# Kernel optimization log

Hardware: AMD Instinct MI355X
Metric: run time of the kernel (lower is better)

Reference implementation:

```python
import jax, jax.numpy as jnp
import numpy as np

VOCAB = 100000
PAD_ID = 0
INTEREST_ID = 1
B, S, D = 16, 200, 128

def setup_inputs() -> dict:
    key = jax.random.key(0)
    ks = jax.random.split(key, 10)
    sc = 0.05
    return {
        "x": jax.random.normal(ks[0], (B, S, D), jnp.float32),
        "x_ids": jax.random.randint(ks[1], (B, S), 0, VOCAB),
        "Wq": jax.random.normal(ks[2], (D, D), jnp.float32) * sc,
        "bq": jax.random.normal(ks[3], (D,), jnp.float32) * sc,
        "Wk": jax.random.normal(ks[4], (D, D), jnp.float32) * sc,
        "bk": jax.random.normal(ks[5], (D,), jnp.float32) * sc,
        "Wv": jax.random.normal(ks[6], (D, 1), jnp.float32) * sc,
        "bv": jax.random.normal(ks[7], (1,), jnp.float32) * sc,
        "Wec": jax.random.normal(ks[8], (2 * D, VOCAB), jnp.float32) * sc,
        "bec": jax.random.normal(ks[9], (VOCAB,), jnp.float32) * sc,
    }

def reference(x, x_ids, Wq, bq, Wk, bk, Wv, bv, Wec, bec):
    # mask: valid (non-pad, non-interest) positions  (B,S)
    mask = (x_ids != PAD_ID) & (x_ids != INTEREST_ID)
    # additive attention pooling (explore_proj=True)
    q = jnp.einsum('bsd,de->bse', x, Wq) + bq            # (B,S,D)
    k = jnp.einsum('bd,de->be', x[:, 0, :], Wk) + bk      # (B,D), broadcast over S
    features = jnp.tanh(q + k[:, None, :])                # (B,S,D)
    scores = jnp.einsum('bsd,do->bso', features, Wv)[..., 0] + bv[0]  # (B,S)
    scores = jax.nn.softmax(scores, axis=-1)
    c_s = jnp.einsum('bsd,bs->bd', x, scores)             # (B,D)
    h_t = x[:, 0, :]                                      # (B,D)
    c_s = jnp.concatenate([h_t, c_s], axis=-1)            # (B,2D)
    p_explore = c_s @ Wec + bec                           # (B,V)
    # explore_mask: histogram of masked ids over vocab.
    # Equivalent to bmm(mask, one_hot(x_ids)) but O(B*S) scatter instead of O(B*S*V).
    explore_mask = jnp.zeros((x.shape[0], VOCAB), jnp.float32)
    batch_idx = jnp.arange(x.shape[0])[:, None]           # (B,1)
    explore_mask = explore_mask.at[batch_idx, x_ids].add(mask.astype(jnp.float32))
    p_explore = jnp.where(explore_mask > 0, -jnp.inf, p_explore)
    return jax.nn.softmax(p_explore, axis=-1)
```

## Files before the change

### kernel.cpp

```cpp
#include <hip/hip_runtime.h>
#include <cstdint>
#include <cstddef>
#include <math.h>

#define B 16
#define S 200
#define D 128
#define VOCAB 100000
#define V4 (VOCAB / 4)
#define SCH 8
#define VTILE 256
#define NBLK ((VOCAB + VTILE - 1) / VTILE)
#define CH 16
#define NCH (2 * D / CH)

__global__ __launch_bounds__(128) void k_scores(
    const float* __restrict__ x,
    const float* __restrict__ Wq, const float* __restrict__ bq,
    const float* __restrict__ Wk, const float* __restrict__ bk,
    const float* __restrict__ Wv, const float* __restrict__ bv,
    float* __restrict__ scores)
{
  const int b  = blockIdx.x / (S / SCH);
  const int s0 = (blockIdx.x % (S / SCH)) * SCH;
  const int e  = threadIdx.x;

  __shared__ float lx[SCH][D];
  __shared__ float l0[D];
  __shared__ float sred[2][SCH];

  l0[e] = x[(size_t)b * S * D + e];
  #pragma unroll
  for (int i = 0; i < SCH; i++) lx[i][e] = x[((size_t)b * S + s0 + i) * D + e];
  __syncthreads();

  float q[SCH];
  const float bqe = bq[e];
  #pragma unroll
  for (int i = 0; i < SCH; i++) q[i] = bqe;
  float kk = bk[e];

  for (int d = 0; d < D; d++) {
    const float wq = Wq[d * D + e];
    const float wk = Wk[d * D + e];
    const float x0 = l0[d];
    kk += x0 * wk;
    #pragma unroll
    for (int i = 0; i < SCH; i++) q[i] += lx[i][d] * wq;
  }

  const float wv  = Wv[e];
  const float bv0 = bv[0];
  #pragma unroll
  for (int i = 0; i < SCH; i++) {
    float val = tanhf(q[i] + kk) * wv;
    #pragma unroll
    for (int off = 32; off > 0; off >>= 1) val += __shfl_down(val, off, 64);
    if ((e & 63) == 0) sred[e >> 6][i] = val;
  }
  __syncthreads();
  if (e < SCH) scores[b * S + s0 + e] = sred[0][e] + sred[1][e] + bv0;
}

__global__ __launch_bounds__(512) void k_csum(
    const float* __restrict__ x, const float* __restrict__ scores,
    float* __restrict__ cvec)
{
  const int b = blockIdx.x;
  const int t = threadIdx.x;
  __shared__ float pr[S];
  __shared__ float redm[9];
  __shared__ float reds[9];
  __shared__ float cpart[3][D];

  float v = (t < S) ? scores[b * S + t] : -INFINITY;
  float m = v;
  #pragma unroll
  for (int off = 32; off > 0; off >>= 1) m = fmaxf(m, __shfl_down(m, off, 64));
  if ((t & 63) == 0) redm[t >> 6] = m;
  __syncthreads();
  if (t == 0) {
    float mm = redm[0];
    #pragma unroll
    for (int i = 1; i < 8; i++) mm = fmaxf(mm, redm[i]);
    redm[8] = mm;
  }
  __syncthreads();
  const float mx = redm[8];

  float e = (t < S) ? expf(v - mx) : 0.f;
  float s = e;
  #pragma unroll
  for (int off = 32; off > 0; off >>= 1) s += __shfl_down(s, off, 64);
  if ((t & 63) == 0) reds[t >> 6] = s;
  __syncthreads();
  if (t == 0) {
    float ss = 0.f;
    #pragma unroll
    for (int i = 0; i < 8; i++) ss += reds[i];
    reds[8] = ss;
  }
  __syncthreads();
  const float inv = 1.0f / reds[8];
  if (t < S) pr[t] = e * inv;
  __syncthreads();

  const int d = t & 127;
  const int sq = t >> 7;
  float acc = 0.f;
  const float* xb = x + ((size_t)b * S + sq * 50) * D + d;
  #pragma unroll 5
  for (int s2 = 0; s2 < 50; s2++) acc += pr[sq * 50 + s2] * xb[s2 * D];
  if (sq) cpart[sq - 1][d] = acc;
  __syncthreads();
  if (sq == 0) {
    cvec[d * B + b]       = x[(size_t)b * S * D + d];
    cvec[(D + d) * B + b] = acc + cpart[0][d] + cpart[1][d] + cpart[2][d];
  }
}

__global__ __launch_bounds__(256, 2) void k_gemv(
    const float* __restrict__ cvec, const float* __restrict__ Wec,
    const float* __restrict__ bec, const int* __restrict__ ids,
    float* __restrict__ out, float* __restrict__ partial)
{
  __shared__ __align__(16) char arena[49152];
  float (*wbuf)[CH][VTILE] = (float (*)[CH][VTILE])arena;
  __shared__ __align__(16) float cl[4096];
  __shared__ unsigned mbit[B * 8];

  const int t    = threadIdx.x;
  const int lane = t & 63;
  const int dq   = __builtin_amdgcn_readfirstlane(t >> 6);

  if (t < B * 8) mbit[t] = 0u;

  const int vbase = blockIdx.x * VTILE;
  const int v4    = blockIdx.x * 64 + lane;
  const bool valid = (v4 < V4);
  const int v4c   = valid ? v4 : (V4 - 1);
  const int laneoff = (vbase + lane * 4 + 3 < VOCAB) ? lane * 4 : 0;

#define STAGE(bufi, c)                                                      \
  { _Pragma("unroll")                                                       \
    for (int r = 0; r < 4; r++) {                                           \
      const int d = (c) * CH + dq * 4 + r;                                  \
      const float* gp = Wec + (size_t)d * VOCAB + vbase + laneoff;          \
      float* lp = &wbuf[bufi][dq * 4 + r][0];                               \
      __builtin_amdgcn_global_load_lds(                                     \
          (const __attribute__((address_space(1))) void*)gp,                \
          (__attribute__((address_space(3))) void*)lp, 16, 0, 0);           \
    } }

#define COMP(bufi, c)                                                      \
  { _Pragma("unroll")                                                      \
    for (int r = 0; r < 4; r++) {                                          \
      const float4 w = ((const float4*)&wbuf[bufi][dq * 4 + r][0])[lane];  \
      const float* cj = cl + ((c) * CH + dq * 4 + r) * 16;                 \
      _Pragma("unroll")                                                    \
      for (int bb = 0; bb < 16; bb++) {                                    \
        const float cc = cj[bb];                                           \
        acc[bb].x = fmaf(w.x, cc, acc[bb].x);                              \
        acc[bb].y = fmaf(w.y, cc, acc[bb].y);                              \
        acc[bb].z = fmaf(w.z, cc, acc[bb].z);                              \
        acc[bb].w = fmaf(w.w, cc, acc[bb].w);                              \
      } } }

  float4 acc[16];
  #pragma unroll
  for (int i = 0; i < 16; i++) acc[i] = make_float4(0.f, 0.f, 0.f, 0.f);

  {
    const float4* src = (const float4*)cvec;
    float4* dst = (float4*)cl;
    #pragma unroll
    for (int i = 0; i < 4; i++) dst[t + 256 * i] = src[t + 256 * i];
  }

  STAGE(0, 0)
  STAGE(1, 1)

  for (int i = t; i < B * S; i += 256) {
    const int id = ids[i];
    if (id > 1 && id >= vbase && id < vbase + VTILE) {
      const int lv = id - vbase;
      atomicOr(&mbit[(i / S) * 8 + (lv >> 5)], 1u << (lv & 31));
    }
  }

  __syncthreads();

  for (int c = 0; c < NCH - 2; c++) {
    STAGE((c + 2) % 3, c + 2)
    asm volatile("s_waitcnt vmcnt(8)" ::: "memory");
    __builtin_amdgcn_sched_barrier(0);
    COMP(c % 3, c)
    __builtin_amdgcn_sched_barrier(0);
  }
  asm volatile("s_waitcnt vmcnt(4)" ::: "memory");
  __builtin_amdgcn_sched_barrier(0);
  COMP((NCH - 2) % 3, NCH - 2)
  asm volatile("s_waitcnt vmcnt(0)" ::: "memory");
  __builtin_amdgcn_sched_barrier(0);
  COMP((NCH - 1) % 3, NCH - 1)

#undef STAGE
#undef COMP

  __syncthreads();

  float2* redp = (float2*)arena;
#define RED(q, l, b) redp[(((q) * 64 + (l)) * 17) + (b)]
#define MASKED(bb, lv) ((mbit[(bb) * 8 + ((lv) >> 5)] >> ((lv) & 31)) & 1u)

  const float4 be4 = ((const float4*)bec)[v4c];
  const int lv0 = lane * 4;
  float psum[4] = {0.f, 0.f, 0.f, 0.f};

  #pragma unroll
  for (int bb = 0; bb < 16; bb++)
    RED(dq, lane, bb) = make_float2(acc[bb].x, acc[bb].y);
  __syncthreads();
  #pragma unroll
  for (int i = 0; i < 4; i++) {
    const int bb = dq * 4 + i;
    const float2 r0 = RED(0, lane, bb), r1 = RED(1, lane, bb);
    const float2 r2 = RED(2, lane, bb), r3 = RED(3, lane, bb);
    const float sx = r0.x + r1.x + r2.x + r3.x;
    const float sy = r0.y + r1.y + r2.y + r3.y;
    float e0 = 0.f, e1 = 0.f;
    if (valid) {
      e0 = MASKED(bb, lv0 + 0) ? 0.f : __expf(sx + be4.x);
      e1 = MASKED(bb, lv0 + 1) ? 0.f : __expf(sy + be4.y);
      *(float2*)&out[(size_t)bb * VOCAB + (size_t)v4 * 4] = make_float2(e0, e1);
    }
    psum[i] += e0 + e1;
  }
  __syncthreads();

  #pragma unroll
  for (int bb = 0; bb < 16; bb++)
    RED(dq, lane, bb) = make_float2(acc[bb].z, acc[bb].w);
  __syncthreads();
  #pragma unroll
  for (int i = 0; i < 4; i++) {
    const int bb = dq * 4 + i;
    const float2 r0 = RED(0, lane, bb), r1 = RED(1, lane, bb);
    const float2 r2 = RED(2, lane, bb), r3 = RED(3, lane, bb);
    const float sz = r0.x + r1.x + r2.x + r3.x;
    const float sw = r0.y + r1.y + r2.y + r3.y;
    float e2 = 0.f, e3 = 0.f;
    if (valid) {
      e2 = MASKED(bb, lv0 + 2) ? 0.f : __expf(sz + be4.z);
      e3 = MASKED(bb, lv0 + 3) ? 0.f : __expf(sw + be4.w);
      *(float2*)&out[(size_t)bb * VOCAB + (size_t)v4 * 4 + 2] = make_float2(e2, e3);
    }
    psum[i] += e2 + e3;
  }
#undef RED
#undef MASKED

  #pragma unroll
  for (int i = 0; i < 4; i++) {
    float s = psum[i];
    #pragma unroll
    for (int off = 32; off > 0; off >>= 1) s += __shfl_down(s, off, 64);
    if (lane == 0) partial[blockIdx.x * 16 + dq * 4 + i] = s;
  }
}

__global__ __launch_bounds__(256) void k_norm(float* __restrict__ out,
                                              const float* __restrict__ partial)
{
  const int b  = blockIdx.y;
  const int t  = threadIdx.x;
  __shared__ float red[4];

  float s = 0.f;
  for (int j = t; j < NBLK; j += 256) s += partial[j * 16 + b];
  #pragma unroll
  for (int off = 32; off > 0; off >>= 1) s += __shfl_down(s, off, 64);
  if ((t & 63) == 0) red[t >> 6] = s;
  __syncthreads();
  const float iv = 1.0f / (red[0] + red[1] + red[2] + red[3]);

  const int i4 = blockIdx.x * 256 + t;
  if (i4 < V4) {
    float4* p = (float4*)out + (size_t)b * V4 + i4;
    float4 q = *p;
    q.x *= iv; q.y *= iv; q.z *= iv; q.w *= iv;
    *p = q;
  }
}

extern "C" void kernel_launch(void* const* d_in, const int* in_sizes, int n_in,
                              void* d_out, int out_size, void* d_ws, size_t ws_size,
                              hipStream_t stream)
{
  const float* x   = (const float*)d_in[0];
  const int*   ids = (const int*)d_in[1];
  const float* Wq  = (const float*)d_in[2];
  const float* bq  = (const float*)d_in[3];
  const float* Wk  = (const float*)d_in[4];
  const float* bk  = (const float*)d_in[5];
  const float* Wv  = (const float*)d_in[6];
  const float* bv  = (const float*)d_in[7];
  const float* Wec = (const float*)d_in[8];
  const float* bec = (const float*)d_in[9];
  float* out = (float*)d_out;
  float* ws  = (float*)d_ws;

  float* scores  = ws;
  float* cvec    = ws + 3200;
  float* partial = ws + 7296;

  k_scores <<<dim3(B * (S / SCH)), dim3(128), 0, stream>>>(x, Wq, bq, Wk, bk, Wv, bv, scores);
  k_csum   <<<dim3(B),             dim3(512), 0, stream>>>(x, scores, cvec);
  k_gemv   <<<dim3(NBLK),          dim3(256), 0, stream>>>(cvec, Wec, bec, ids, out, partial);
  k_norm   <<<dim3((V4 + 255) / 256, B), dim3(256), 0, stream>>>(out, partial);
}
```

Baseline: 56.21 us.

## Replace LDS-staged Wec pipeline with register double-buffered direct loads

The GEMV kernel no longer stages Wec tiles into shared memory through global_load_lds with a triple-buffered waitcnt pipeline. Each wavefront now owns a 64-row slice of the reduction dimension and loads Wec float4s straight into two register buffers, alternating loads and FMAs. The c vector is read from global memory instead of a shared-memory copy. With less shared memory used, launch bounds rise to 3 blocks per CU for more occupancy, at the cost of register pressure from 16 extra float4 buffers and uncached global reads of cvec.

```diff
diff --git a/kernel.cpp b/kernel.cpp
--- a/kernel.cpp
+++ b/kernel.cpp
@@ -11,8 +11,6 @@
 #define SCH 8
 #define VTILE 256
 #define NBLK ((VOCAB + VTILE - 1) / VTILE)
-#define CH 16
-#define NCH (2 * D / CH)
 
 __global__ __launch_bounds__(128) void k_scores(
     const float* __restrict__ x,
@@ -119,14 +117,12 @@
   }
 }
 
-__global__ __launch_bounds__(256, 2) void k_gemv(
+__global__ __launch_bounds__(256, 3) void k_gemv(
     const float* __restrict__ cvec, const float* __restrict__ Wec,
     const float* __restrict__ bec, const int* __restrict__ ids,
     float* __restrict__ out, float* __restrict__ partial)
 {
-  __shared__ __align__(16) char arena[49152];
-  float (*wbuf)[CH][VTILE] = (float (*)[CH][VTILE])arena;
-  __shared__ __align__(16) float cl[4096];
+  __shared__ float2 red[4][64][17];
   __shared__ unsigned mbit[B * 8];
 
   const int t    = threadIdx.x;
@@ -139,24 +135,34 @@
   const int v4    = blockIdx.x * 64 + lane;
   const bool valid = (v4 < V4);
   const int v4c   = valid ? v4 : (V4 - 1);
-  const int laneoff = (vbase + lane * 4 + 3 < VOCAB) ? lane * 4 : 0;
-
-#define STAGE(bufi, c)                                                      \
-  { _Pragma("unroll")                                                       \
-    for (int r = 0; r < 4; r++) {                                           \
-      const int d = (c) * CH + dq * 4 + r;                                  \
-      const float* gp = Wec + (size_t)d * VOCAB + vbase + laneoff;          \
-      float* lp = &wbuf[bufi][dq * 4 + r][0];                               \
-      __builtin_amdgcn_global_load_lds(                                     \
-          (const __attribute__((address_space(1))) void*)gp,                \
-          (__attribute__((address_space(3))) void*)lp, 16, 0, 0);           \
-    } }
-
-#define COMP(bufi, c)                                                      \
+  const int dbase = dq * 64;
+
+  const float4* wp = (const float4*)Wec + (size_t)dbase * V4 + v4c;
+  const float*  cp = cvec + dbase * 16;
+
+  for (int i = t; i < B * S; i += 256) {
+    const int id = ids[i];
+    if (id > 1 && id >= vbase && id < vbase + VTILE) {
+      const int lv = id - vbase;
+      atomicOr(&mbit[(i / S) * 8 + (lv >> 5)], 1u << (lv & 31));
+    }
+  }
+
+  float4 acc[16];
+  #pragma unroll
+  for (int i = 0; i < 16; i++) acc[i] = make_float4(0.f, 0.f, 0.f, 0.f);
+
+  float4 wa[8], wb[8];
+
+#define LOADW(buf, c0)                                                     \
   { _Pragma("unroll")                                                      \
-    for (int r = 0; r < 4; r++) {                                          \
-      const float4 w = ((const float4*)&wbuf[bufi][dq * 4 + r][0])[lane];  \
-      const float* cj = cl + ((c) * CH + dq * 4 + r) * 16;                 \
+    for (int j = 0; j < 8; j++) buf[j] = wp[(size_t)((c0) * 8 + j) * V4]; }
+
+#define COMPW(buf, c0)                                                     \
+  { _Pragma("unroll")                                                      \
+    for (int j = 0; j < 8; j++) {                                          \
+      const float* cj = cp + ((c0) * 8 + j) * 16;   \
+      const float4 w = buf[j];                                             \
       _Pragma("unroll")                                                    \
       for (int bb = 0; bb < 16; bb++) {                                    \
         const float cc = cj[bb];                                           \
@@ -166,51 +172,29 @@
         acc[bb].w = fmaf(w.w, cc, acc[bb].w);                              \
       } } }
 
-  float4 acc[16];
-  #pragma unroll
-  for (int i = 0; i < 16; i++) acc[i] = make_float4(0.f, 0.f, 0.f, 0.f);
-
-  {
-    const float4* src = (const float4*)cvec;
-    float4* dst = (float4*)cl;
-    #pragma unroll
-    for (int i = 0; i < 4; i++) dst[t + 256 * i] = src[t + 256 * i];
-  }
-
-  STAGE(0, 0)
-  STAGE(1, 1)
-
-  for (int i = t; i < B * S; i += 256) {
-    const int id = ids[i];
-    if (id > 1 && id >= vbase && id < vbase + VTILE) {
-      const int lv = id - vbase;
-      atomicOr(&mbit[(i / S) * 8 + (lv >> 5)], 1u << (lv & 31));
-    }
-  }
-
-  __syncthreads();
-
-  for (int c = 0; c < NCH - 2; c++) {
-    STAGE((c + 2) % 3, c + 2)
-    asm volatile("s_waitcnt vmcnt(8)" ::: "memory");
-    __builtin_amdgcn_sched_barrier(0);
-    COMP(c % 3, c)
-    __builtin_amdgcn_sched_barrier(0);
-  }
-  asm volatile("s_waitcnt vmcnt(4)" ::: "memory");
-  __builtin_amdgcn_sched_barrier(0);
-  COMP((NCH - 2) % 3, NCH - 2)
-  asm volatile("s_waitcnt vmcnt(0)" ::: "memory");
-  __builtin_amdgcn_sched_barrier(0);
-  COMP((NCH - 1) % 3, NCH - 1)
-
-#undef STAGE
-#undef COMP
-
-  __syncthreads();
-
-  float2* redp = (float2*)arena;
-#define RED(q, l, b) redp[(((q) * 64 + (l)) * 17) + (b)]
+  LOADW(wa, 0)
+  LOADW(wb, 1)
+  COMPW(wa, 0)
+  LOADW(wa, 2)
+  COMPW(wb, 1)
+  LOADW(wb, 3)
+  COMPW(wa, 2)
+  LOADW(wa, 4)
+  COMPW(wb, 3)
+  LOADW(wb, 5)
+  COMPW(wa, 4)
+  LOADW(wa, 6)
+  COMPW(wb, 5)
+  LOADW(wb, 7)
+  COMPW(wa, 6)
+  COMPW(wb, 7)
+
+#undef LOADW
+#undef COMPW
+
+  __syncthreads();
+
+#define RED(q, l, b) red[q][l][b]
 #define MASKED(bb, lv) ((mbit[(bb) * 8 + ((lv) >> 5)] >> ((lv) & 31)) & 1u)
 
   const float4 be4 = ((const float4*)bec)[v4c];
```

Result: slower. 67.72 us (+20.5%).
